# Kernel tuning notes

Measured on AMD Instinct MI355X. Metric: run time of the kernel, lower is better.

The kernel has to match this reference:

```python
import jax, jax.numpy as jnp
import numpy as np

S = 3000    # number of candidate spans (rows of g_i)
P = 80000   # total (mention, antecedent) pairs
GI = 768    # gi_dim
DD = 20     # distance/genre/speaker embedding dim
HID = 150   # mlp hidden dim (fixed in source)
ORDER = 2   # N: one higher-order refinement pass


def setup_inputs() -> dict:
    key = jax.random.key(0)
    ks = jax.random.split(key, 18)
    gij = 3 * GI + 3 * DD
    g_i = jax.random.normal(ks[0], (S, GI), jnp.float32)
    mention_scores = jax.random.normal(ks[1], (S, 1), jnp.float32)
    # sorted segment ids: ragged antecedent counts per mention, grouped contiguously
    mention_ids = jnp.sort(jax.random.randint(ks[2], (P,), 0, S, dtype=jnp.int32))
    antecedent_ids = jax.random.randint(ks[3], (P,), 0, S, dtype=jnp.int32)
    dist_bins = jax.random.randint(ks[4], (P,), 0, 10, dtype=jnp.int32)
    genre_ids = jax.random.randint(ks[5], (P,), 0, 7, dtype=jnp.int32) + 1   # 1..7, 0 is padding_idx
    speaker_ids = jax.random.randint(ks[6], (P,), 0, 2, dtype=jnp.int32) + 1  # 1..2, 0 is padding_idx
    w = lambda k, shp: 0.02 * jax.random.normal(k, shp, jnp.float32)
    dist_emb = w(ks[7], (10, DD))
    genre_emb = w(ks[8], (8, DD)).at[0].set(0.0)     # padding_idx=0
    speaker_emb = w(ks[9], (3, DD)).at[0].set(0.0)   # padding_idx=0
    W1 = w(ks[10], (gij, HID)); b1 = jnp.zeros((HID,), jnp.float32)
    W2 = w(ks[11], (HID, HID)); b2 = jnp.zeros((HID,), jnp.float32)
    W3 = w(ks[12], (HID, 1)); b3 = jnp.zeros((1,), jnp.float32)
    Wf = w(ks[13], (2 * GI, 1)); bf = jnp.zeros((1,), jnp.float32)
    return {"g_i": g_i, "mention_scores": mention_scores, "mention_ids": mention_ids,
            "antecedent_ids": antecedent_ids, "dist_bins": dist_bins, "genre_ids": genre_ids,
            "speaker_ids": speaker_ids, "dist_emb": dist_emb, "genre_emb": genre_emb,
            "speaker_emb": speaker_emb, "W1": W1, "b1": b1, "W2": W2, "b2": b2,
            "W3": W3, "b3": b3, "Wf": Wf, "bf": bf}


def _mlp(x, W1, b1, W2, b2, W3, b3):
    h = jax.nn.relu(x @ W1 + b1)
    h = jax.nn.relu(h @ W2 + b2)
    return h @ W3 + b3


def reference(g_i, mention_scores, mention_ids, antecedent_ids, dist_bins, genre_ids,
              speaker_ids, dist_emb, genre_emb, speaker_emb, W1, b1, W2, b2, W3, b3, Wf, bf):
    phi = jnp.concatenate([dist_emb[dist_bins], genre_emb[genre_ids], speaker_emb[speaker_ids]], axis=1)  # [P,60]
    seg = dict(num_segments=S, indices_are_sorted=True)
    g = g_i
    scores = None
    for n in range(ORDER):
        i_g = g[mention_ids]                # [P,GI] gather
        j_g = g[antecedent_ids]             # [P,GI] gather
        pairs = jnp.concatenate([i_g, j_g, i_g * j_g, phi], axis=1)  # [P,gij]
        scores = _mlp(pairs, W1, b1, W2, b2, W3, b3)                 # [P,1]
        if n < ORDER - 1:
            # higher_order_refinement: ragged segment softmax + weighted scatter update
            s = scores[:, 0]
            seg_max = jax.ops.segment_max(s, mention_ids, **seg)
            safe_max = jnp.where(jnp.isfinite(seg_max), seg_max, 0.0)
            e = jnp.exp(s - safe_max[mention_ids])
            denom = jax.ops.segment_sum(e, mention_ids, **seg)
            attn = e / jnp.where(denom > 0, denom, 1.0)[mention_ids]
            weighted = jax.ops.segment_sum(attn[:, None] * j_g, mention_ids, **seg)  # [S,GI]
            counts = jax.ops.segment_sum(jnp.ones_like(s), mention_ids, **seg)
            f = jax.nn.sigmoid(jnp.concatenate([g, weighted], axis=1) @ Wf + bf)  # [S,1]
            # NOTE: faithful to the source bug: f * mention_id (the integer index), not f * mention_g
            ids_f = jnp.arange(S, dtype=g.dtype)[:, None]
            g_new = f * ids_f + (1.0 - f) * weighted
            g = jnp.where(counts[:, None] > 0, g_new, g)
    s_i = mention_scores[mention_ids]
    s_j = mention_scores[antecedent_ids]
    coref_scores = s_i + s_j + scores       # [P,1]
    # segment softmax with an extra epsilon (score 0) logit per mention
    c = coref_scores[:, 0]
    seg_max = jax.ops.segment_max(c, mention_ids, **seg)
    m = jnp.maximum(jnp.where(jnp.isfinite(seg_max), seg_max, 0.0), 0.0)  # include epsilon logit 0
    e = jnp.exp(c - m[mention_ids])
    denom = jax.ops.segment_sum(e, mention_ids, **seg) + jnp.exp(-m)
    pair_probs = e / denom[mention_ids]     # [P]
    eps_probs = jnp.exp(-m) / denom         # [S]
    return coref_scores, pair_probs, eps_probs
```

## Files before the change

### kernel.cpp

```cpp
#include <hip/hip_runtime.h>

#define GI   768
#define HID  150
#define HPAD 160
#define DDIM 20

typedef __attribute__((ext_vector_type(8))) short v8s;
typedef __attribute__((ext_vector_type(16))) float f32x16;

#define MFMA(A, B, C) __builtin_amdgcn_mfma_f32_32x32x16_bf16(A, B, C, 0, 0, 0)

__device__ __forceinline__ ushort bf16rn(float x) {
  unsigned u = __float_as_uint(x);
  return (ushort)((u + 0x7fffu + ((u >> 16) & 1u)) >> 16);
}
__device__ __forceinline__ void bsplit(float x, ushort& h, ushort& l) {
  h = bf16rn(x);
  float fh = __uint_as_float((unsigned)h << 16);
  l = bf16rn(x - fh);
}
__device__ __forceinline__ uint4 pack8(const ushort* v) {
  uint4 r;
  r.x = v[0] | ((unsigned)v[1] << 16); r.y = v[2] | ((unsigned)v[3] << 16);
  r.z = v[4] | ((unsigned)v[5] << 16); r.w = v[6] | ((unsigned)v[7] << 16);
  return r;
}

__device__ __forceinline__ int qoffb(int row, int kb) {
  return row * 96 + (kb ^ (((row >> 2) & 3) << 4));
}
__device__ __forceinline__ int hoffb(int row, int kb) {
  return row * 336 + (kb ^ (((row >> 3) & 3) << 4));
}

__global__ void seg_kernel(const int* __restrict__ mI, int* __restrict__ segs,
                           int P, int S) {
  int m = blockIdx.x * 256 + threadIdx.x;
  if (m > S) return;
  int lo = 0, hi = P;
  while (lo < hi) { int mid = (lo + hi) >> 1; if (mI[mid] < m) lo = mid + 1; else hi = mid; }
  segs[m] = lo;
}

__global__ void phi_kernel(const float* __restrict__ de, const float* __restrict__ ge,
                           const float* __restrict__ se, const float* __restrict__ W1,
                           float* __restrict__ phiW) {
  int idx = blockIdx.x * 256 + threadIdx.x;
  if (idx >= 21 * HPAD) return;
  int row = idx / HPAD, h = idx % HPAD;
  float v = 0.f;
  if (h < HID) {
    const float* emb; int off;
    if (row < 10)      { emb = de + row * DDIM;        off = 0; }
    else if (row < 18) { emb = ge + (row - 10) * DDIM; off = DDIM; }
    else               { emb = se + (row - 18) * DDIM; off = 2 * DDIM; }
    for (int k = 0; k < DDIM; ++k) v += emb[k] * W1[(3 * GI + off + k) * HID + h];
  }
  phiW[row * HPAD + h] = v;
}

__global__ void pad2_kernel(const float* __restrict__ W1, const float* __restrict__ W2,
                            const float* __restrict__ b1, const float* __restrict__ b2,
                            const float* __restrict__ W3,
                            ushort* __restrict__ WThi, ushort* __restrict__ WTlo,
                            ushort* __restrict__ W2Thi, ushort* __restrict__ W2Tlo,
                            float* __restrict__ b1p, float* __restrict__ b2p,
                            float* __restrict__ W3p) {
  int idx = blockIdx.x * 256 + threadIdx.x;
  if (idx < 480 * GI) {
    int c = idx / GI, r = idx % GI;
    int seg = c / HPAD, h = c % HPAD;
    float x = (h < HID) ? W1[(size_t)(seg * GI + r) * HID + h] : 0.f;
    ushort hh, ll; bsplit(x, hh, ll);
    WThi[idx] = hh; WTlo[idx] = ll; return;
  }
  idx -= 480 * GI;
  if (idx < HPAD * HPAD) {
    int c = idx / HPAD, k = idx % HPAD;
    float x = (c < HID && k < HID) ? W2[(size_t)k * HID + c] : 0.f;
    ushort hh, ll; bsplit(x, hh, ll);
    W2Thi[idx] = hh; W2Tlo[idx] = ll; return;
  }
  idx -= HPAD * HPAD;
  if (idx < HPAD) { b1p[idx] = (idx < HID) ? b1[idx] : 0.f; return; }
  idx -= HPAD;
  if (idx < HPAD) { b2p[idx] = (idx < HID) ? b2[idx] : 0.f; return; }
  idx -= HPAD;
  if (idx < HPAD) { W3p[idx] = (idx < HID) ? W3[idx] : 0.f; return; }
}

__global__ __launch_bounds__(320, 4) void pre2_kernel(
    const float* __restrict__ g, const ushort* __restrict__ WThi,
    const ushort* __restrict__ WTlo, float* __restrict__ pre, int S) {
  __shared__ char pool[24576];
  const int t = threadIdx.x;
  const int lane = t & 63, w = t >> 6;
  const int lcol = lane & 31, half = lane >> 5;
  const int row0 = blockIdx.x * 64;
  const int hb = blockIdx.y * HPAD;

  f32x16 acc0 = {}, acc1 = {};
  const ushort* wh = WThi + (size_t)(hb + w * 32 + lcol) * GI + 8 * half;
  const ushort* wl = WTlo + (size_t)(hb + w * 32 + lcol) * GI + 8 * half;

  const int qr = (t < 256) ? (t >> 2) : 0;
  const int qob = qoffb(qr, (t & 3) * 16);
  int srow = row0 + qr; if (srow >= S) srow = S - 1;
  const float* gp = g + (size_t)srow * GI + (t & 3) * 8;

  if (t < 256) {
    float4 a0 = *(const float4*)(gp), a1 = *(const float4*)(gp + 4);
    float xr[8] = {a0.x, a0.y, a0.z, a0.w, a1.x, a1.y, a1.z, a1.w};
    ushort hs[8], ls[8];
#pragma unroll
    for (int j = 0; j < 8; ++j) bsplit(xr[j], hs[j], ls[j]);
    *(uint4*)(pool + qob) = pack8(hs);
    *(uint4*)(pool + 6144 + qob) = pack8(ls);
  }
  v8s cwh0 = *(const v8s*)(wh), cwh1 = *(const v8s*)(wh + 16);
  v8s cwl0 = *(const v8s*)(wl), cwl1 = *(const v8s*)(wl + 16);
  __syncthreads();

  int cur = 0;
#pragma unroll 1
  for (int d0 = 0; d0 < GI; d0 += 32) {
    const bool has = (d0 + 32) < GI;
    const int dn = has ? d0 + 32 : 0;
    float4 na0, na1;
    if (t < 256) { na0 = *(const float4*)(gp + dn); na1 = *(const float4*)(gp + dn + 4); }
    v8s nwh0 = *(const v8s*)(wh + dn), nwh1 = *(const v8s*)(wh + dn + 16);
    v8s nwl0 = *(const v8s*)(wl + dn), nwl1 = *(const v8s*)(wl + dn + 16);

    const char* qh = pool + cur * 12288;
    const char* ql = qh + 6144;
    {
      const int kb = 16 * half;
      v8s a0h = *(const v8s*)(qh + qoffb(lcol, kb));
      v8s a0l = *(const v8s*)(ql + qoffb(lcol, kb));
      acc0 = MFMA(a0h, cwh0, acc0); acc0 = MFMA(a0l, cwh0, acc0); acc0 = MFMA(a0h, cwl0, acc0);
      v8s a1h = *(const v8s*)(qh + qoffb(32 + lcol, kb));
      v8s a1l = *(const v8s*)(ql + qoffb(32 + lcol, kb));
      acc1 = MFMA(a1h, cwh0, acc1); acc1 = MFMA(a1l, cwh0, acc1); acc1 = MFMA(a1h, cwl0, acc1);
    }
    {
      const int kb = 32 + 16 * half;
      v8s a0h = *(const v8s*)(qh + qoffb(lcol, kb));
      v8s a0l = *(const v8s*)(ql + qoffb(lcol, kb));
      acc0 = MFMA(a0h, cwh1, acc0); acc0 = MFMA(a0l, cwh1, acc0); acc0 = MFMA(a0h, cwl1, acc0);
      v8s a1h = *(const v8s*)(qh + qoffb(32 + lcol, kb));
      v8s a1l = *(const v8s*)(ql + qoffb(32 + lcol, kb));
      acc1 = MFMA(a1h, cwh1, acc1); acc1 = MFMA(a1l, cwh1, acc1); acc1 = MFMA(a1h, cwl1, acc1);
    }
    if (has && t < 256) {
      float xr[8] = {na0.x, na0.y, na0.z, na0.w, na1.x, na1.y, na1.z, na1.w};
      ushort hs[8], ls[8];
#pragma unroll
      for (int j = 0; j < 8; ++j) bsplit(xr[j], hs[j], ls[j]);
      char* dst = pool + (cur ^ 1) * 12288;
      *(uint4*)(dst + qob) = pack8(hs);
      *(uint4*)(dst + 6144 + qob) = pack8(ls);
    }
    cwh0 = nwh0; cwh1 = nwh1; cwl0 = nwl0; cwl1 = nwl1;
    __syncthreads();
    cur ^= 1;
  }

  const int h = w * 32 + lcol;
#pragma unroll
  for (int q = 0; q < 16; ++q) {
    int p = (q & 3) + 8 * (q >> 2) + 4 * half;
    int s0 = row0 + p;
    if (s0 < S) pre[(size_t)s0 * 320 + hb + h] = acc0[q];
    int s1 = row0 + 32 + p;
    if (s1 < S) pre[(size_t)s1 * 320 + hb + h] = acc1[q];
  }
}

__global__ __launch_bounds__(320, 4) void h1s_kernel(
    const float* __restrict__ g, const float* __restrict__ pre,
    const float* __restrict__ phiW,
    const ushort* __restrict__ WThi, const ushort* __restrict__ WTlo,
    const ushort* __restrict__ W2Thi, const ushort* __restrict__ W2Tlo,
    const float* __restrict__ b1p, const float* __restrict__ b2p,
    const float* __restrict__ W3p, const float* __restrict__ b3,
    const int* __restrict__ mI, const int* __restrict__ aI,
    const int* __restrict__ db, const int* __restrict__ ge, const int* __restrict__ sp,
    float* __restrict__ sOut, int P) {
  __shared__ char pool[43008];
  __shared__ int sIi[64], sIj[64], sRd[64], sRg[64], sRs[64];
  __shared__ float sRed[64];
  ushort* thi = (ushort*)pool;
  ushort* tlo = thi + 64 * 168;

  const int t = threadIdx.x;
  const int lane = t & 63, w = t >> 6;
  const int lcol = lane & 31, half = lane >> 5;
  const int p0 = blockIdx.x * 64;

  if (t < 64) {
    int p = p0 + t;
    sIi[t] = mI[p]; sIj[t] = aI[p];
    sRd[t] = db[p]; sRg[t] = 10 + ge[p]; sRs[t] = 18 + sp[p];
    sRed[t] = 0.f;
  }

  f32x16 acc0 = {}, acc1 = {};
  const ushort* wh = WThi + (size_t)(320 + w * 32 + lcol) * GI + 8 * half;
  const ushort* wl = WTlo + (size_t)(320 + w * 32 + lcol) * GI + 8 * half;

  __syncthreads();

  const int qr = (t < 256) ? (t >> 2) : 0;
  const int qob = qoffb(qr, (t & 3) * 16);
  const float* gi = g + (size_t)sIi[qr] * GI + (t & 3) * 8;
  const float* gj = g + (size_t)sIj[qr] * GI + (t & 3) * 8;

  if (t < 256) {
    float4 a0 = *(const float4*)(gi), a1 = *(const float4*)(gi + 4);
    float4 b0 = *(const float4*)(gj), b1v = *(const float4*)(gj + 4);
    float xr[8] = {a0.x * b0.x, a0.y * b0.y, a0.z * b0.z, a0.w * b0.w,
                   a1.x * b1v.x, a1.y * b1v.y, a1.z * b1v.z, a1.w * b1v.w};
    ushort hs[8], ls[8];
#pragma unroll
    for (int j = 0; j < 8; ++j) bsplit(xr[j], hs[j], ls[j]);
    *(uint4*)(pool + qob) = pack8(hs);
    *(uint4*)(pool + 6144 + qob) = pack8(ls);
  }
  v8s cwh0 = *(const v8s*)(wh), cwh1 = *(const v8s*)(wh + 16);
  v8s cwl0 = *(const v8s*)(wl), cwl1 = *(const v8s*)(wl + 16);
  __syncthreads();

  int cur = 0;
#pragma unroll 1
  for (int d0 = 0; d0 < GI; d0 += 32) {
    const bool has = (d0 + 32) < GI;
    const int dn = has ? d0 + 32 : 0;
    float4 na0, na1, nb0, nb1;
    if (t < 256) {
      na0 = *(const float4*)(gi + dn); na1 = *(const float4*)(gi + dn + 4);
      nb0 = *(const float4*)(gj + dn); nb1 = *(const float4*)(gj + dn + 4);
    }
    v8s nwh0 = *(const v8s*)(wh + dn), nwh1 = *(const v8s*)(wh + dn + 16);
    v8s nwl0 = *(const v8s*)(wl + dn), nwl1 = *(const v8s*)(wl + dn + 16);

    const char* qh = pool + cur * 12288;
    const char* ql = qh + 6144;
    {
      const int kb = 16 * half;
      v8s a0h = *(const v8s*)(qh + qoffb(lcol, kb));
      v8s a0l = *(const v8s*)(ql + qoffb(lcol, kb));
      acc0 = MFMA(a0h, cwh0, acc0); acc0 = MFMA(a0l, cwh0, acc0); acc0 = MFMA(a0h, cwl0, acc0);
      v8s a1h = *(const v8s*)(qh + qoffb(32 + lcol, kb));
      v8s a1l = *(const v8s*)(ql + qoffb(32 + lcol, kb));
      acc1 = MFMA(a1h, cwh0, acc1); acc1 = MFMA(a1l, cwh0, acc1); acc1 = MFMA(a1h, cwl0, acc1);
    }
    {
      const int kb = 32 + 16 * half;
      v8s a0h = *(const v8s*)(qh + qoffb(lcol, kb));
      v8s a0l = *(const v8s*)(ql + qoffb(lcol, kb));
      acc0 = MFMA(a0h, cwh1, acc0); acc0 = MFMA(a0l, cwh1, acc0); acc0 = MFMA(a0h, cwl1, acc0);
      v8s a1h = *(const v8s*)(qh + qoffb(32 + lcol, kb));
      v8s a1l = *(const v8s*)(ql + qoffb(32 + lcol, kb));
      acc1 = MFMA(a1h, cwh1, acc1); acc1 = MFMA(a1l, cwh1, acc1); acc1 = MFMA(a1h, cwl1, acc1);
    }
    if (has && t < 256) {
      float xr[8] = {na0.x * nb0.x, na0.y * nb0.y, na0.z * nb0.z, na0.w * nb0.w,
                     na1.x * nb1.x, na1.y * nb1.y, na1.z * nb1.z, na1.w * nb1.w};
      ushort hs[8], ls[8];
#pragma unroll
      for (int j = 0; j < 8; ++j) bsplit(xr[j], hs[j], ls[j]);
      char* dst = pool + (cur ^ 1) * 12288;
      *(uint4*)(dst + qob) = pack8(hs);
      *(uint4*)(dst + 6144 + qob) = pack8(ls);
    }
    cwh0 = nwh0; cwh1 = nwh1; cwl0 = nwl0; cwl1 = nwl1;
    __syncthreads();
    cur ^= 1;
  }

  const int h = w * 32 + lcol;
  const float b1v = b1p[h];
#pragma unroll
  for (int q = 0; q < 16; ++q) {
    const int rr = (q & 3) + 8 * (q >> 2) + 4 * half;
    {
      int p = rr;
      float v = acc0[q] + b1v
              + pre[(size_t)sIi[p] * 320 + h] + pre[(size_t)sIj[p] * 320 + 160 + h]
              + phiW[sRd[p] * HPAD + h] + phiW[sRg[p] * HPAD + h] + phiW[sRs[p] * HPAD + h];
      v = fmaxf(v, 0.f);
      ushort hh, ll; bsplit(v, hh, ll);
      *(ushort*)((char*)thi + hoffb(p, 2 * h)) = hh;
      *(ushort*)((char*)tlo + hoffb(p, 2 * h)) = ll;
    }
    {
      int p = 32 + rr;
      float v = acc1[q] + b1v
              + pre[(size_t)sIi[p] * 320 + h] + pre[(size_t)sIj[p] * 320 + 160 + h]
              + phiW[sRd[p] * HPAD + h] + phiW[sRg[p] * HPAD + h] + phiW[sRs[p] * HPAD + h];
      v = fmaxf(v, 0.f);
      ushort hh, ll; bsplit(v, hh, ll);
      *(ushort*)((char*)thi + hoffb(p, 2 * h)) = hh;
      *(ushort*)((char*)tlo + hoffb(p, 2 * h)) = ll;
    }
  }
  __syncthreads();

  f32x16 c0 = {}, c1 = {};
  const ushort* u2h = W2Thi + (size_t)(w * 32 + lcol) * HPAD + 8 * half;
  const ushort* u2l = W2Tlo + (size_t)(w * 32 + lcol) * HPAD + 8 * half;
#pragma unroll
  for (int c = 0; c < HPAD; c += 32) {
#pragma unroll
    for (int kh = 0; kh < 2; ++kh) {
      v8s bh = *(const v8s*)(u2h + c + 16 * kh);
      v8s bl = *(const v8s*)(u2l + c + 16 * kh);
      const int kb = 2 * (c + 16 * kh) + 16 * half;
      v8s a0h = *(const v8s*)((char*)thi + hoffb(lcol, kb));
      v8s a0l = *(const v8s*)((char*)tlo + hoffb(lcol, kb));
      c0 = MFMA(a0h, bh, c0); c0 = MFMA(a0l, bh, c0); c0 = MFMA(a0h, bl, c0);
      v8s a1h = *(const v8s*)((char*)thi + hoffb(32 + lcol, kb));
      v8s a1l = *(const v8s*)((char*)tlo + hoffb(32 + lcol, kb));
      c1 = MFMA(a1h, bh, c1); c1 = MFMA(a1l, bh, c1); c1 = MFMA(a1h, bl, c1);
    }
  }

  const float b2v = b2p[h], w3v = W3p[h];
#pragma unroll
  for (int q = 0; q < 16; ++q) {
    float v0 = fmaxf(c0[q] + b2v, 0.f) * w3v;
    float v1 = fmaxf(c1[q] + b2v, 0.f) * w3v;
#pragma unroll
    for (int m = 16; m; m >>= 1) {
      v0 += __shfl_xor(v0, m, 32);
      v1 += __shfl_xor(v1, m, 32);
    }
    if (lcol == 0) {
      const int rr = (q & 3) + 8 * (q >> 2) + 4 * half;
      atomicAdd(&sRed[rr], v0);
      atomicAdd(&sRed[32 + rr], v1);
    }
  }
  __syncthreads();
  if (t < 64) sOut[p0 + t] = sRed[t] + b3[0];
}

__global__ void mid_kernel(const float* __restrict__ g, const float* __restrict__ s1,
                           const int* __restrict__ segs, const int* __restrict__ aI,
                           const float* __restrict__ Wf, const float* __restrict__ bf,
                           float* __restrict__ g2) {
  const int m = blockIdx.x;
  const int t = threadIdx.x;
  const int st = segs[m], en = segs[m + 1], n = en - st;
  if (n == 0) {
    for (int d = t; d < GI; d += 256) g2[m * GI + d] = g[m * GI + d];
    return;
  }
  __shared__ float red[256];
  float mx = -INFINITY;
  for (int p = st + t; p < en; p += 256) mx = fmaxf(mx, s1[p]);
  red[t] = mx; __syncthreads();
  for (int s = 128; s > 0; s >>= 1) { if (t < s) red[t] = fmaxf(red[t], red[t + s]); __syncthreads(); }
  mx = red[0]; __syncthreads();
  float sm = 0.f;
  for (int p = st + t; p < en; p += 256) sm += expf(s1[p] - mx);
  red[t] = sm; __syncthreads();
  for (int s = 128; s > 0; s >>= 1) { if (t < s) red[t] += red[t + s]; __syncthreads(); }
  const float denom = red[0]; __syncthreads();
  float wv[3] = {0.f, 0.f, 0.f};
  for (int p = st; p < en; ++p) {
    float e = expf(s1[p] - mx);
    const float* gj = g + (size_t)aI[p] * GI;
#pragma unroll
    for (int u = 0; u < 3; ++u) wv[u] += e * gj[t + u * 256];
  }
#pragma unroll
  for (int u = 0; u < 3; ++u) wv[u] /= denom;
  float part = 0.f;
#pragma unroll
  for (int u = 0; u < 3; ++u) {
    int d = t + u * 256;
    part += g[m * GI + d] * Wf[d] + wv[u] * Wf[GI + d];
  }
  red[t] = part; __syncthreads();
  for (int s = 128; s > 0; s >>= 1) { if (t < s) red[t] += red[t + s]; __syncthreads(); }
  const float f = 1.f / (1.f + expf(-(red[0] + bf[0])));
#pragma unroll
  for (int u = 0; u < 3; ++u) {
    int d = t + u * 256;
    g2[m * GI + d] = f * (float)m + (1.f - f) * wv[u];
  }
}

__global__ void coref_kernel(const float* __restrict__ ms, const float* __restrict__ s2,
                             const int* __restrict__ mI, const int* __restrict__ aI,
                             float* __restrict__ out, int P) {
  int p = blockIdx.x * 256 + threadIdx.x;
  if (p >= P) return;
  out[p] = ms[mI[p]] + ms[aI[p]] + s2[p];
}

__global__ void final_kernel(const float* __restrict__ c, const int* __restrict__ segs,
                             float* __restrict__ pairP, float* __restrict__ epsP) {
  const int m = blockIdx.x;
  const int t = threadIdx.x;
  const int st = segs[m], en = segs[m + 1], n = en - st;
  __shared__ float red[256];
  float mx = -INFINITY;
  for (int p = st + t; p < en; p += 256) mx = fmaxf(mx, c[p]);
  red[t] = mx; __syncthreads();
  for (int s = 128; s > 0; s >>= 1) { if (t < s) red[t] = fmaxf(red[t], red[t + s]); __syncthreads(); }
  mx = red[0]; __syncthreads();
  const float m2 = (n > 0) ? fmaxf(mx, 0.f) : 0.f;
  float sm = 0.f;
  for (int p = st + t; p < en; p += 256) sm += expf(c[p] - m2);
  red[t] = sm; __syncthreads();
  for (int s = 128; s > 0; s >>= 1) { if (t < s) red[t] += red[t + s]; __syncthreads(); }
  const float denom = red[0] + expf(-m2);
  for (int p = st + t; p < en; p += 256) pairP[p] = expf(c[p] - m2) / denom;
  if (t == 0) epsP[m] = expf(-m2) / denom;
}

extern "C" void kernel_launch(void* const* d_in, const int* in_sizes, int n_in,
                              void* d_out, int out_size, void* d_ws, size_t ws_size,
                              hipStream_t stream) {
  const float* g_i  = (const float*)d_in[0];
  const float* ms   = (const float*)d_in[1];
  const int*   mI   = (const int*)d_in[2];
  const int*   aI   = (const int*)d_in[3];
  const int*   db   = (const int*)d_in[4];
  const int*   ge   = (const int*)d_in[5];
  const int*   sp   = (const int*)d_in[6];
  const float* de   = (const float*)d_in[7];
  const float* gemb = (const float*)d_in[8];
  const float* semb = (const float*)d_in[9];
  const float* W1   = (const float*)d_in[10];
  const float* b1   = (const float*)d_in[11];
  const float* W2   = (const float*)d_in[12];
  const float* b2   = (const float*)d_in[13];
  const float* W3   = (const float*)d_in[14];
  const float* b3   = (const float*)d_in[15];
  const float* Wf   = (const float*)d_in[16];
  const float* bf   = (const float*)d_in[17];

  const int S = in_sizes[0] / GI;
  const int P = in_sizes[2];
  float* out = (float*)d_out;

  char* ws = (char*)d_ws;
  size_t off = 0;
  auto take = [&](size_t bytes) -> char* {
    char* p = ws + off;
    off = (off + bytes + 15) & ~(size_t)15;
    return p;
  };
  int*    segs  = (int*)   take((size_t)(S + 1) * 4);
  float*  phiW  = (float*) take((size_t)21 * HPAD * 4);
  float*  pre   = (float*) take((size_t)S * 320 * 4);
  float*  g2    = (float*) take((size_t)S * GI * 4);
  float*  s1    = (float*) take((size_t)P * 4);
  float*  s2    = (float*) take((size_t)P * 4);
  ushort* WThi  = (ushort*)take((size_t)480 * GI * 2);
  ushort* WTlo  = (ushort*)take((size_t)480 * GI * 2);
  ushort* W2Thi = (ushort*)take((size_t)HPAD * HPAD * 2);
  ushort* W2Tlo = (ushort*)take((size_t)HPAD * HPAD * 2);
  float*  b1p   = (float*) take((size_t)HPAD * 4);
  float*  b2p   = (float*) take((size_t)HPAD * 4);
  float*  W3p   = (float*) take((size_t)HPAD * 4);

  const int gridSeg = (S + 1 + 255) / 256;
  const int gridPhi = (21 * HPAD + 255) / 256;
  const int gridPad = (480 * GI + HPAD * HPAD + 3 * HPAD + 255) / 256;
  const dim3 gridPre((S + 63) / 64, 2);
  const int gridH   = P / 64;
  const int gridCor = (P + 255) / 256;

  seg_kernel<<<gridSeg, 256, 0, stream>>>(mI, segs, P, S);
  phi_kernel<<<gridPhi, 256, 0, stream>>>(de, gemb, semb, W1, phiW);
  pad2_kernel<<<gridPad, 256, 0, stream>>>(W1, W2, b1, b2, W3,
                                           WThi, WTlo, W2Thi, W2Tlo, b1p, b2p, W3p);

  pre2_kernel<<<gridPre, 320, 0, stream>>>(g_i, WThi, WTlo, pre, S);
  h1s_kernel<<<gridH, 320, 0, stream>>>(g_i, pre, phiW, WThi, WTlo, W2Thi, W2Tlo,
                                        b1p, b2p, W3p, b3, mI, aI, db, ge, sp, s1, P);
  mid_kernel<<<S, 256, 0, stream>>>(g_i, s1, segs, aI, Wf, bf, g2);

  pre2_kernel<<<gridPre, 320, 0, stream>>>(g2, WThi, WTlo, pre, S);
  h1s_kernel<<<gridH, 320, 0, stream>>>(g2, pre, phiW, WThi, WTlo, W2Thi, W2Tlo,
                                        b1p, b2p, W3p, b3, mI, aI, db, ge, sp, s2, P);

  coref_kernel<<<gridCor, 256, 0, stream>>>(ms, s2, mI, aI, out, P);
  final_kernel<<<S, 256, 0, stream>>>(out, segs, out + P, out + 2 * (size_t)P);
}
```

Before: 449.2 us.

## Split pair MLP into single-wave h1 and score kernels with pre-swizzled weights

Replaces the fused 320-thread pair-MLP kernel with two 64-thread kernels. The first computes the first hidden layer for 32 pairs per wave, reading g rows straight into MFMA operands and weights from a fragment-ordered layout with no LDS or barriers, then writes h1 as hi/lo bf16 to global memory. The second runs the W2 layer and the W3 dot product. It also swaps round-to-nearest splitting for cheaper truncation splitting. The aim is to drop LDS staging and syncs, at the cost of an extra 2x P×160 global round trip and weights reloaded per wave, with truncation slightly changing numerics.

```diff
diff --git a/kernel.cpp b/kernel.cpp
--- a/kernel.cpp
+++ b/kernel.cpp
@@ -18,6 +18,12 @@
   h = bf16rn(x);
   float fh = __uint_as_float((unsigned)h << 16);
   l = bf16rn(x - fh);
+}
+__device__ __forceinline__ void tsplit(float x, ushort& h, ushort& l) {
+  unsigned u = __float_as_uint(x);
+  h = (ushort)(u >> 16);
+  float d = x - __uint_as_float(u & 0xffff0000u);
+  l = (ushort)(__float_as_uint(d) >> 16);
 }
 __device__ __forceinline__ uint4 pack8(const ushort* v) {
   uint4 r;
@@ -25,12 +31,14 @@
   r.z = v[4] | ((unsigned)v[5] << 16); r.w = v[6] | ((unsigned)v[7] << 16);
   return r;
 }
+__device__ __forceinline__ v8s mk8(const ushort* v) {
+  union { uint4 u; v8s s; } t;
+  t.u = pack8(v);
+  return t.s;
+}
 
 __device__ __forceinline__ int qoffb(int row, int kb) {
   return row * 96 + (kb ^ (((row >> 2) & 3) << 4));
-}
-__device__ __forceinline__ int hoffb(int row, int kb) {
-  return row * 336 + (kb ^ (((row >> 3) & 3) << 4));
 }
 
 __global__ void seg_kernel(const int* __restrict__ mI, int* __restrict__ segs,
@@ -63,9 +71,9 @@
                             const float* __restrict__ b1, const float* __restrict__ b2,
                             const float* __restrict__ W3,
                             ushort* __restrict__ WThi, ushort* __restrict__ WTlo,
-                            ushort* __restrict__ W2Thi, ushort* __restrict__ W2Tlo,
-                            float* __restrict__ b1p, float* __restrict__ b2p,
-                            float* __restrict__ W3p) {
+                            ushort* __restrict__ WBhi, ushort* __restrict__ WBlo,
+                            ushort* __restrict__ W2Bhi, ushort* __restrict__ W2Blo,
+                            float* __restrict__ b1p, float2* __restrict__ b2w3) {
   int idx = blockIdx.x * 256 + threadIdx.x;
   if (idx < 480 * GI) {
     int c = idx / GI, r = idx % GI;
@@ -75,18 +83,34 @@
     WThi[idx] = hh; WTlo[idx] = ll; return;
   }
   idx -= 480 * GI;
-  if (idx < HPAD * HPAD) {
-    int c = idx / HPAD, k = idx % HPAD;
-    float x = (c < HID && k < HID) ? W2[(size_t)k * HID + c] : 0.f;
+  if (idx < 5 * 48 * 512) {
+    int c = idx / (48 * 512); int r1 = idx % (48 * 512);
+    int s = r1 / 512; int r2 = r1 % 512;
+    int l = r2 / 8, j = r2 % 8;
+    int h = c * 32 + (l & 31);
+    int k = s * 16 + 8 * (l >> 5) + j;
+    float x = (h < HID) ? W1[(size_t)(2 * GI + k) * HID + h] : 0.f;
     ushort hh, ll; bsplit(x, hh, ll);
-    W2Thi[idx] = hh; W2Tlo[idx] = ll; return;
-  }
-  idx -= HPAD * HPAD;
+    WBhi[idx] = hh; WBlo[idx] = ll; return;
+  }
+  idx -= 5 * 48 * 512;
+  if (idx < 5 * 10 * 512) {
+    int rt = idx / (10 * 512); int r1 = idx % (10 * 512);
+    int s = r1 / 512; int r2 = r1 % 512;
+    int l = r2 / 8, j = r2 % 8;
+    int h2 = rt * 32 + (l & 31);
+    int k = s * 16 + 8 * (l >> 5) + j;
+    float x = (k < HID && h2 < HID) ? W2[(size_t)k * HID + h2] : 0.f;
+    ushort hh, ll; bsplit(x, hh, ll);
+    W2Bhi[idx] = hh; W2Blo[idx] = ll; return;
+  }
+  idx -= 5 * 10 * 512;
   if (idx < HPAD) { b1p[idx] = (idx < HID) ? b1[idx] : 0.f; return; }
   idx -= HPAD;
-  if (idx < HPAD) { b2p[idx] = (idx < HID) ? b2[idx] : 0.f; return; }
-  idx -= HPAD;
-  if (idx < HPAD) { W3p[idx] = (idx < HID) ? W3[idx] : 0.f; return; }
+  if (idx < HPAD) {
+    b2w3[idx] = make_float2((idx < HID) ? b2[idx] : 0.f, (idx < HID) ? W3[idx] : 0.f);
+    return;
+  }
 }
 
 __global__ __launch_bounds__(320, 4) void pre2_kernel(
@@ -176,173 +200,124 @@
   }
 }
 
-__global__ __launch_bounds__(320, 4) void h1s_kernel(
+__global__ __launch_bounds__(64, 3) void h1a_kernel(
     const float* __restrict__ g, const float* __restrict__ pre,
     const float* __restrict__ phiW,
-    const ushort* __restrict__ WThi, const ushort* __restrict__ WTlo,
-    const ushort* __restrict__ W2Thi, const ushort* __restrict__ W2Tlo,
-    const float* __restrict__ b1p, const float* __restrict__ b2p,
-    const float* __restrict__ W3p, const float* __restrict__ b3,
+    const ushort* __restrict__ WBhi, const ushort* __restrict__ WBlo,
+    const float* __restrict__ b1p,
     const int* __restrict__ mI, const int* __restrict__ aI,
     const int* __restrict__ db, const int* __restrict__ ge, const int* __restrict__ sp,
-    float* __restrict__ sOut, int P) {
-  __shared__ char pool[43008];
-  __shared__ int sIi[64], sIj[64], sRd[64], sRg[64], sRs[64];
-  __shared__ float sRed[64];
-  ushort* thi = (ushort*)pool;
-  ushort* tlo = thi + 64 * 168;
-
-  const int t = threadIdx.x;
-  const int lane = t & 63, w = t >> 6;
+    ushort* __restrict__ h1hi, ushort* __restrict__ h1lo, int P) {
+  const int lane = threadIdx.x;
   const int lcol = lane & 31, half = lane >> 5;
-  const int p0 = blockIdx.x * 64;
-
-  if (t < 64) {
-    int p = p0 + t;
-    sIi[t] = mI[p]; sIj[t] = aI[p];
-    sRd[t] = db[p]; sRg[t] = 10 + ge[p]; sRs[t] = 18 + sp[p];
-    sRed[t] = 0.f;
-  }
-
-  f32x16 acc0 = {}, acc1 = {};
-  const ushort* wh = WThi + (size_t)(320 + w * 32 + lcol) * GI + 8 * half;
-  const ushort* wl = WTlo + (size_t)(320 + w * 32 + lcol) * GI + 8 * half;
-
-  __syncthreads();
-
-  const int qr = (t < 256) ? (t >> 2) : 0;
-  const int qob = qoffb(qr, (t & 3) * 16);
-  const float* gi = g + (size_t)sIi[qr] * GI + (t & 3) * 8;
-  const float* gj = g + (size_t)sIj[qr] * GI + (t & 3) * 8;
-
-  if (t < 256) {
-    float4 a0 = *(const float4*)(gi), a1 = *(const float4*)(gi + 4);
-    float4 b0 = *(const float4*)(gj), b1v = *(const float4*)(gj + 4);
+  const int p0 = blockIdx.x * 32;
+
+  const int myp = p0 + lcol;
+  const int iA = mI[myp], jA = aI[myp];
+  const int rdL = db[myp], rgL = 10 + ge[myp], rsL = 18 + sp[myp];
+
+  const float* gi = g + (size_t)iA * GI + 8 * half;
+  const float* gj = g + (size_t)jA * GI + 8 * half;
+
+  f32x16 acc[5];
+  {
+    f32x16 z = {};
+#pragma unroll
+    for (int c = 0; c < 5; ++c) acc[c] = z;
+  }
+
+#pragma unroll 2
+  for (int s = 0; s < 48; ++s) {
+    const int d0 = s * 16;
+    const float4 a0 = *(const float4*)(gi + d0);
+    const float4 a1 = *(const float4*)(gi + d0 + 4);
+    const float4 b0 = *(const float4*)(gj + d0);
+    const float4 b1v = *(const float4*)(gj + d0 + 4);
     float xr[8] = {a0.x * b0.x, a0.y * b0.y, a0.z * b0.z, a0.w * b0.w,
                    a1.x * b1v.x, a1.y * b1v.y, a1.z * b1v.z, a1.w * b1v.w};
     ushort hs[8], ls[8];
 #pragma unroll
-    for (int j = 0; j < 8; ++j) bsplit(xr[j], hs[j], ls[j]);
-    *(uint4*)(pool + qob) = pack8(hs);
-    *(uint4*)(pool + 6144 + qob) = pack8(ls);
-  }
-  v8s cwh0 = *(const v8s*)(wh), cwh1 = *(const v8s*)(wh + 16);
-  v8s cwl0 = *(const v8s*)(wl), cwl1 = *(const v8s*)(wl + 16);
-  __syncthreads();
-
-  int cur = 0;
-#pragma unroll 1
-  for (int d0 = 0; d0 < GI; d0 += 32) {
-    const bool has = (d0 + 32) < GI;
-    const int dn = has ? d0 + 32 : 0;
-    float4 na0, na1, nb0, nb1;
-    if (t < 256) {
-      na0 = *(const float4*)(gi + dn); na1 = *(const float4*)(gi + dn + 4);
-      nb0 = *(const float4*)(gj + dn); nb1 = *(const float4*)(gj + dn + 4);
-    }
-    v8s nwh0 = *(const v8s*)(wh + dn), nwh1 = *(const v8s*)(wh + dn + 16);
-    v8s nwl0 = *(const v8s*)(wl + dn), nwl1 = *(const v8s*)(wl + dn + 16);
-
-    const char* qh = pool + cur * 12288;
-    const char* ql = qh + 6144;
-    {
-      const int kb = 16 * half;
-      v8s a0h = *(const v8s*)(qh + qoffb(lcol, kb));
-      v8s a0l = *(const v8s*)(ql + qoffb(lcol, kb));
-      acc0 = MFMA(a0h, cwh0, acc0); acc0 = MFMA(a0l, cwh0, acc0); acc0 = MFMA(a0h, cwl0, acc0);
-      v8s a1h = *(const v8s*)(qh + qoffb(32 + lcol, kb));
-      v8s a1l = *(const v8s*)(ql + qoffb(32 + lcol, kb));
-      acc1 = MFMA(a1h, cwh0, acc1); acc1 = MFMA(a1l, cwh0, acc1); acc1 = MFMA(a1h, cwl0, acc1);
-    }
-    {
-      const int kb = 32 + 16 * half;
-      v8s a0h = *(const v8s*)(qh + qoffb(lcol, kb));
-      v8s a0l = *(const v8s*)(ql + qoffb(lcol, kb));
-      acc0 = MFMA(a0h, cwh1, acc0); acc0 = MFMA(a0l, cwh1, acc0); acc0 = MFMA(a0h, cwl1, acc0);
-      v8s a1h = *(const v8s*)(qh + qoffb(32 + lcol, kb));
-      v8s a1l = *(const v8s*)(ql + qoffb(32 + lcol, kb));
-      acc1 = MFMA(a1h, cwh1, acc1); acc1 = MFMA(a1l, cwh1, acc1); acc1 = MFMA(a1h, cwl1, acc1);
-    }
-    if (has && t < 256) {
-      float xr[8] = {na0.x * nb0.x, na0.y * nb0.y, na0.z * nb0.z, na0.w * nb0.w,
-                     na1.x * nb1.x, na1.y * nb1.y, na1.z * nb1.z, na1.w * nb1.w};
-      ushort hs[8], ls[8];
-#pragma unroll
-      for (int j = 0; j < 8; ++j) bsplit(xr[j], hs[j], ls[j]);
-      char* dst = pool + (cur ^ 1) * 12288;
-      *(uint4*)(dst + qob) = pack8(hs);
-      *(uint4*)(dst + 6144 + qob) = pack8(ls);
-    }
-    cwh0 = nwh0; cwh1 = nwh1; cwl0 = nwl0; cwl1 = nwl1;
-    __syncthreads();
-    cur ^= 1;
-  }
-
-  const int h = w * 32 + lcol;
-  const float b1v = b1p[h];
+    for (int j = 0; j < 8; ++j) tsplit(xr[j], hs[j], ls[j]);
+    const v8s ah = mk8(hs), al = mk8(ls);
+#pragma unroll
+    for (int c = 0; c < 5; ++c) {
+      const size_t o = ((size_t)(c * 48 + s) * 64 + lane) * 8;
+      const v8s bh = *(const v8s*)(WBhi + o);
+      const v8s bl = *(const v8s*)(WBlo + o);
+      acc[c] = MFMA(ah, bh, acc[c]);
+      acc[c] = MFMA(al, bh, acc[c]);
+      acc[c] = MFMA(ah, bl, acc[c]);
+    }
+  }
+
 #pragma unroll
   for (int q = 0; q < 16; ++q) {
     const int rr = (q & 3) + 8 * (q >> 2) + 4 * half;
-    {
-      int p = rr;
-      float v = acc0[q] + b1v
-              + pre[(size_t)sIi[p] * 320 + h] + pre[(size_t)sIj[p] * 320 + 160 + h]
-              + phiW[sRd[p] * HPAD + h] + phiW[sRg[p] * HPAD + h] + phiW[sRs[p] * HPAD + h];
+    const int pI = __shfl(iA, rr);
+    const int pJ = __shfl(jA, rr);
+    const int rd = __shfl(rdL, rr), rg = __shfl(rgL, rr), rs = __shfl(rsL, rr);
+    const float* preI = pre + (size_t)pI * 320;
+    const float* preJ = pre + (size_t)pJ * 320 + 160;
+    const size_t prow = (size_t)(p0 + rr) * 160;
+#pragma unroll
+    for (int c = 0; c < 5; ++c) {
+      const int col = c * 32 + lcol;
+      float v = acc[c][q] + b1p[col] + preI[col] + preJ[col]
+              + phiW[rd * HPAD + col] + phiW[rg * HPAD + col] + phiW[rs * HPAD + col];
       v = fmaxf(v, 0.f);
-      ushort hh, ll; bsplit(v, hh, ll);
-      *(ushort*)((char*)thi + hoffb(p, 2 * h)) = hh;
-      *(ushort*)((char*)tlo + hoffb(p, 2 * h)) = ll;
-    }
-    {
-      int p = 32 + rr;
-      float v = acc1[q] + b1v
-              + pre[(size_t)sIi[p] * 320 + h] + pre[(size_t)sIj[p] * 320 + 160 + h]
-              + phiW[sRd[p] * HPAD + h] + phiW[sRg[p] * HPAD + h] + phiW[sRs[p] * HPAD + h];
-      v = fmaxf(v, 0.f);
-      ushort hh, ll; bsplit(v, hh, ll);
-      *(ushort*)((char*)thi + hoffb(p, 2 * h)) = hh;
-      *(ushort*)((char*)tlo + hoffb(p, 2 * h)) = ll;
-    }
-  }
-  __syncthreads();
-
-  f32x16 c0 = {}, c1 = {};
-  const ushort* u2h = W2Thi + (size_t)(w * 32 + lcol) * HPAD + 8 * half;
-  const ushort* u2l = W2Tlo + (size_t)(w * 32 + lcol) * HPAD + 8 * half;
-#pragma unroll
-  for (int c = 0; c < HPAD; c += 32) {
-#pragma unroll
-    for (int kh = 0; kh < 2; ++kh) {
-      v8s bh = *(const v8s*)(u2h + c + 16 * kh);
-      v8s bl = *(const v8s*)(u2l + c + 16 * kh);
-      const int kb = 2 * (c + 16 * kh) + 16 * half;
-      v8s a0h = *(const v8s*)((char*)thi + hoffb(lcol, kb));
-      v8s a0l = *(const v8s*)((char*)tlo + hoffb(lcol, kb));
-      c0 = MFMA(a0h, bh, c0); c0 = MFMA(a0l, bh, c0); c0 = MFMA(a0h, bl, c0);
-      v8s a1h = *(const v8s*)((char*)thi + hoffb(32 + lcol, kb));
-      v8s a1l = *(const v8s*)((char*)tlo + hoffb(32 + lcol, kb));
-      c1 = MFMA(a1h, bh, c1); c1 = MFMA(a1l, bh, c1); c1 = MFMA(a1h, bl, c1);
-    }
-  }
-
-  const float b2v = b2p[h], w3v = W3p[h];
-#pragma unroll
-  for (int q = 0; q < 16; ++q) {
-    float v0 = fmaxf(c0[q] + b2v, 0.f) * w3v;
-    float v1 = fmaxf(c1[q] + b2v, 0.f) * w3v;
-#pragma unroll
-    for (int m = 16; m; m >>= 1) {
-      v0 += __shfl_xor(v0, m, 32);
-      v1 += __shfl_xor(v1, m, 32);
-    }
-    if (lcol == 0) {
-      const int rr = (q & 3) + 8 * (q >> 2) + 4 * half;
-      atomicAdd(&sRed[rr], v0);
-      atomicAdd(&sRed[32 + rr], v1);
-    }
-  }
-  __syncthreads();
-  if (t < 64) sOut[p0 + t] = sRed[t] + b3[0];
+      ushort hh, ll; tsplit(v, hh, ll);
+      h1hi[prow + col] = hh;
+      h1lo[prow + col] = ll;
+    }
+  }
+}
+
+__global__ __launch_bounds__(64, 3) void score3_kernel(
+    const ushort* __restrict__ h1hi, const ushort* __restrict__ h1lo,
+    const ushort* __restrict__ W2Bhi, const ushort* __restrict__ W2Blo,
+    const float2* __restrict__ b2w3, const float* __restrict__ b3,
+    float* __restrict__ sOut, int P) {
+  const int lane = threadIdx.x;
+  const int lcol = lane & 31, half = lane >> 5;
+  const int p0 = blockIdx.x * 32;
+
+  const ushort* hh = h1hi + (size_t)(p0 + lcol) * 160 + 8 * half;
+  const ushort* hl = h1lo + (size_t)(p0 + lcol) * 160 + 8 * half;
+
+  f32x16 acc[5];
+  {
+    f32x16 z = {};
+#pragma unroll
+    for (int r = 0; r < 5; ++r) acc[r] = z;
+  }
+
+#pragma unroll 2
+  for (int s = 0; s < 10; ++s) {
+    const v8s bh = *(const v8s*)(hh + s * 16);
+    const v8s bl = *(const v8s*)(hl + s * 16);
+#pragma unroll
+    for (int r = 0; r < 5; ++r) {
+      const size_t o = ((size_t)(r * 10 + s) * 64 + lane) * 8;
+      const v8s ah = *(const v8s*)(W2Bhi + o);
+      const v8s al = *(const v8s*)(W2Blo + o);
+      acc[r] = MFMA(ah, bh, acc[r]);
+      acc[r] = MFMA(al, bh, acc[r]);
+      acc[r] = MFMA(ah, bl, acc[r]);
+    }
+  }
+
+  float part = 0.f;
+#pragma unroll
+  for (int r = 0; r < 5; ++r) {
+#pragma unroll
+    for (int q = 0; q < 16; ++q) {
+      const int h2 = r * 32 + (q & 3) + 8 * (q >> 2) + 4 * half;
+      const float2 bw = b2w3[h2];
+      part += fmaxf(acc[r][q] + bw.x, 0.f) * bw.y;
+    }
+  }
+  part += __shfl_xor(part, 32);
+  if (lane < 32) sOut[p0 + lane] = part + b3[0];
 }
 
 __global__ void mid_kernel(const float* __restrict__ g, const float* __restrict__ s1,
@@ -462,32 +437,38 @@
   float*  s2    = (float*) take((size_t)P * 4);
   ushort* WThi  = (ushort*)take((size_t)480 * GI * 2);
   ushort* WTlo  = (ushort*)take((size_t)480 * GI * 2);
-  ushort* W2Thi = (ushort*)take((size_t)HPAD * HPAD * 2);
-  ushort* W2Tlo = (ushort*)take((size_t)HPAD * HPAD * 2);
+  ushort* WBhi  = (ushort*)take((size_t)5 * 48 * 512 * 2);
+  ushort* WBlo  = (ushort*)take((size_t)5 * 48 * 512 * 2);
+  ushort* W2Bhi = (ushort*)take((size_t)5 * 10 * 512 * 2);
+  ushort* W2Blo = (ushort*)take((size_t)5 * 10 * 512 * 2);
   float*  b1p   = (float*) take((size_t)HPAD * 4);
-  float*  b2p   = (float*) take((size_t)HPAD * 4);
-  float*  W3p   = (float*) take((size_t)HPAD * 4);
+  float2* b2w3  = (float2*)take((size_t)HPAD * 8);
+  ushort* h1hi  = (ushort*)take((size_t)P * 160 * 2);
+  ushort* h1lo  = (ushort*)take((size_t)P * 160 * 2);
 
   const int gridSeg = (S + 1 + 255) / 256;
   const int gridPhi = (21 * HPAD + 255) / 256;
-  const int gridPad = (480 * GI + HPAD * HPAD + 3 * HPAD + 255) / 256;
+  const int padTot  = 480 * GI + 5 * 48 * 512 + 5 * 10 * 512 + 2 * HPAD;
+  const int gridPad = (padTot + 255) / 256;
   const dim3 gridPre((S + 63) / 64, 2);
-  const int gridH   = P / 64;
+  const int gridH   = P / 32;
   const int gridCor = (P + 255) / 256;
 
   seg_kernel<<<gridSeg, 256, 0, stream>>>(mI, segs, P, S);
   phi_kernel<<<gridPhi, 256, 0, stream>>>(de, gemb, semb, W1, phiW);
-  pad2_kernel<<<gridPad, 256, 0, stream>>>(W1, W2, b1, b2, W3,
-                                           WThi, WTlo, W2Thi, W2Tlo, b1p, b2p, W3p);
+  pad2_kernel<<<gridPad, 256, 0, stream>>>(W1, W2, b1, b2, W3, WThi, WTlo,
+                                           WBhi, WBlo, W2Bhi, W2Blo, b1p, b2w3);
 
   pre2_kernel<<<gridPre, 320, 0, stream>>>(g_i, WThi, WTlo, pre, S);
-  h1s_kernel<<<gridH, 320, 0, stream>>>(g_i, pre, phiW, WThi, WTlo, W2Thi, W2Tlo,
-                                        b1p, b2p, W3p, b3, mI, aI, db, ge, sp, s1, P);
+  h1a_kernel<<<gridH, 64, 0, stream>>>(g_i, pre, phiW, WBhi, WBlo, b1p,
+                                       mI, aI, db, ge, sp, h1hi, h1lo, P);
+  score3_kernel<<<gridH, 64, 0, stream>>>(h1hi, h1lo, W2Bhi, W2Blo, b2w3, b3, s1, P);
   mid_kernel<<<S, 256, 0, stream>>>(g_i, s1, segs, aI, Wf, bf, g2);
 
   pre2_kernel<<<gridPre, 320, 0, stream>>>(g2, WThi, WTlo, pre, S);
-  h1s_kernel<<<gridH, 320, 0, stream>>>(g2, pre, phiW, WThi, WTlo, W2Thi, W2Tlo,
-                                        b1p, b2p, W3p, b3, mI, aI, db, ge, sp, s2, P);
+  h1a_kernel<<<gridH, 64, 0, stream>>>(g2, pre, phiW, WBhi, WBlo, b1p,
+                                       mI, aI, db, ge, sp, h1hi, h1lo, P);
+  score3_kernel<<<gridH, 64, 0, stream>>>(h1hi, h1lo, W2Bhi, W2Blo, b2w3, b3, s2, P);
 
   coref_kernel<<<gridCor, 256, 0, stream>>>(ms, s2, mI, aI, out, P);
   final_kernel<<<S, 256, 0, stream>>>(out, segs, out + P, out + 2 * (size_t)P);
```

Measured after the change: 397.6 us. 11.5% less time.
